# Optimization experiments

Hardware: AMD Instinct MI355X
Metric: run time of the kernel (lower is better)

The kernel has to match this reference:

```python
import jax, jax.numpy as jnp
import numpy as np

N, D, H, E, K = 16384, 1024, 4096, 8, 2
EPS = 1e-5


def setup_inputs() -> dict:
    key = jax.random.key(0)
    ks = jax.random.split(key, 12)
    s = 0.02
    return {
        "x": jax.random.normal(ks[0], (N, D), dtype=jnp.float32),
        "ln_g": jnp.ones((D,), jnp.float32),
        "ln_b": jnp.zeros((D,), jnp.float32),
        "r_w1": jax.random.normal(ks[1], (D, H // 2), jnp.float32) * s,
        "r_b1": jnp.zeros((H // 2,), jnp.float32),
        "r_w2": jax.random.normal(ks[2], (H // 2, E), jnp.float32) * s,
        "r_b2": jnp.zeros((E,), jnp.float32),
        "e_w1": jax.random.normal(ks[3], (E, D, H), jnp.float32) * s,
        "e_b1": jnp.zeros((E, H), jnp.float32),
        "e_w2": jax.random.normal(ks[4], (E, H, D), jnp.float32) * s,
        "e_b2": jnp.zeros((E, D), jnp.float32),
    }


def reference(x, ln_g, ln_b, r_w1, r_b1, r_w2, r_b2, e_w1, e_b1, e_w2, e_b2):
    # LayerNorm
    mu = jnp.mean(x, axis=-1, keepdims=True)
    var = jnp.mean(jnp.square(x - mu), axis=-1, keepdims=True)
    xn = (x - mu) * jax.lax.rsqrt(var + EPS) * ln_g + ln_b  # [N, D]

    # Router: Linear -> ReLU -> Linear -> softmax -> top-k, renormalize
    logits = jax.nn.relu(xn @ r_w1 + r_b1) @ r_w2 + r_b2  # [N, E]
    probs = jax.nn.softmax(logits, axis=-1)
    vals, idx = jax.lax.top_k(probs, K)  # [N, K]
    vals = vals / jnp.sum(vals, axis=-1, keepdims=True)

    # Dense expert dispatch: loop over fixed small E, weight by combine gate
    out = jnp.zeros_like(x)
    for e in range(E):
        gate = jnp.sum(vals * (idx == e).astype(vals.dtype), axis=-1)  # [N]
        h = jax.nn.relu(xn @ e_w1[e] + e_b1[e])  # dropout in eval mode -> identity
        y = h @ e_w2[e] + e_b2[e]  # [N, D]
        out = out + gate[:, None] * y
    return x + out
```

## Files before the change

kernel.cpp:

```cpp
#include <hip/hip_runtime.h>
#include <cstdint>
#include <cstddef>

typedef unsigned short u16;
typedef __attribute__((ext_vector_type(8))) short bf16x8;
typedef __attribute__((ext_vector_type(4))) float f32x4;

#define N_TOK 16384
#define DIM   1024
#define HID   4096
#define NEXP  8
#define HR    2048
#define TAU   0.02f
#define MAXMT 264
#define MAXMT2 136

__device__ __forceinline__ u16 f2bf(float f) {
  union { float f; uint32_t u; } x; x.f = f;
  uint32_t r = x.u + 0x7FFFu + ((x.u >> 16) & 1u);
  return (u16)(r >> 16);
}
__device__ __forceinline__ float bf2f(u16 u) {
  union { uint32_t u; float f; } x; x.u = ((uint32_t)u) << 16; return x.f;
}

__device__ __forceinline__ void async16(const void* g, const void* l) {
  auto gp = reinterpret_cast<const __attribute__((address_space(1))) uint32_t*>(
      reinterpret_cast<uintptr_t>(g));
  auto lp = reinterpret_cast<__attribute__((address_space(3))) uint32_t*>(
      reinterpret_cast<uintptr_t>(l));
  __builtin_amdgcn_global_load_lds(gp, lp, 16, 0, 0);
}

__device__ __forceinline__ unsigned xcd_swz(unsigned flat, unsigned nwg) {
  const unsigned xcd = flat & 7u, lid = flat >> 3;
  const unsigned q = nwg >> 3, r = nwg & 7u;
  return (xcd < r ? xcd * (q + 1u) : r * (q + 1u) + (xcd - r) * q) + lid;
}

template<bool SPLIT>
__global__ __launch_bounds__(256)
void transpose_cvt(const float* __restrict__ src, u16* __restrict__ hi,
                   u16* __restrict__ lo, int R, int C)
{
  __shared__ float tile[64][65];
  const size_t bofs = (size_t)blockIdx.z * R * C;
  src += bofs; hi += bofs; if (SPLIT) lo += bofs;
  const int t = threadIdx.x;
  const int c0 = blockIdx.x * 64, r0 = blockIdx.y * 64;
#pragma unroll
  for (int i = 0; i < 4; ++i) {
    const int idx = i * 256 + t;
    const int rr = idx >> 4;
    const int cc = (idx & 15) << 2;
    const float4 v = *(const float4*)(src + (size_t)(r0 + rr) * C + c0 + cc);
    tile[rr][cc] = v.x; tile[rr][cc + 1] = v.y;
    tile[rr][cc + 2] = v.z; tile[rr][cc + 3] = v.w;
  }
  __syncthreads();
#pragma unroll
  for (int i = 0; i < 4; ++i) {
    const int idx = i * 256 + t;
    const int oc = idx >> 4;
    const int rc = (idx & 15) << 2;
    float v0 = tile[rc][oc], v1 = tile[rc + 1][oc];
    float v2 = tile[rc + 2][oc], v3 = tile[rc + 3][oc];
    ushort4 h;
    h.x = f2bf(v0); h.y = f2bf(v1); h.z = f2bf(v2); h.w = f2bf(v3);
    const size_t o = (size_t)(c0 + oc) * R + r0 + rc;
    *(ushort4*)(hi + o) = h;
    if (SPLIT) {
      ushort4 l;
      l.x = f2bf(v0 - bf2f(h.x)); l.y = f2bf(v1 - bf2f(h.y));
      l.z = f2bf(v2 - bf2f(h.z)); l.w = f2bf(v3 - bf2f(h.w));
      *(ushort4*)(lo + o) = l;
    }
  }
}

__global__ __launch_bounds__(256)
void ln_kernel(const float* __restrict__ x, const float* __restrict__ g,
               const float* __restrict__ b, u16* __restrict__ xh,
               u16* __restrict__ xl, float* __restrict__ out)
{
  const int row = blockIdx.x;
  const int t = threadIdx.x;
  const float4 xv = ((const float4*)(x + (size_t)row * DIM))[t];
  float s = xv.x + xv.y + xv.z + xv.w;
  float q = xv.x * xv.x + xv.y * xv.y + xv.z * xv.z + xv.w * xv.w;
#pragma unroll
  for (int off = 32; off; off >>= 1) {
    s += __shfl_down(s, off, 64);
    q += __shfl_down(q, off, 64);
  }
  __shared__ float sm[8];
  __shared__ float mu_s, rs_s;
  const int lane = t & 63, wv = t >> 6;
  if (lane == 0) { sm[wv] = s; sm[wv + 4] = q; }
  __syncthreads();
  if (t == 0) {
    float S = sm[0] + sm[1] + sm[2] + sm[3];
    float Q = sm[4] + sm[5] + sm[6] + sm[7];
    float mu = S * (1.f / DIM);
    float var = Q * (1.f / DIM) - mu * mu;
    mu_s = mu; rs_s = rsqrtf(var + 1e-5f);
  }
  __syncthreads();
  const float mu = mu_s, rs = rs_s;
  const float4 gv = ((const float4*)g)[t];
  const float4 bv = ((const float4*)b)[t];
  float n0 = (xv.x - mu) * rs * gv.x + bv.x;
  float n1 = (xv.y - mu) * rs * gv.y + bv.y;
  float n2 = (xv.z - mu) * rs * gv.z + bv.z;
  float n3 = (xv.w - mu) * rs * gv.w + bv.w;
  ushort4 h, l;
  h.x = f2bf(n0); l.x = f2bf(n0 - bf2f(h.x));
  h.y = f2bf(n1); l.y = f2bf(n1 - bf2f(h.y));
  h.z = f2bf(n2); l.z = f2bf(n2 - bf2f(h.z));
  h.w = f2bf(n3); l.w = f2bf(n3 - bf2f(h.w));
  ((ushort4*)(xh + (size_t)row * DIM))[t] = h;
  ((ushort4*)(xl + (size_t)row * DIM))[t] = l;
  ((float4*)(out + (size_t)row * DIM))[t] = xv;
}

__global__ __launch_bounds__(256)
void logits_kernel(const u16* __restrict__ HrB, const float* __restrict__ w2,
                   float* __restrict__ logits)
{
  const int row = blockIdx.x, t = threadIdx.x;
  const u16* h = HrB + (size_t)row * HR;
  const ushort4* hv = (const ushort4*)(h + t * 8);
  ushort4 h0 = hv[0], h1 = hv[1];
  u16 hh[8] = {h0.x, h0.y, h0.z, h0.w, h1.x, h1.y, h1.z, h1.w};
  float p[8] = {0, 0, 0, 0, 0, 0, 0, 0};
#pragma unroll
  for (int j = 0; j < 8; ++j) {
    const int col = t * 8 + j;
    const float v = bf2f(hh[j]);
    const float4* wp = (const float4*)(w2 + (size_t)col * 8);
    float4 a = wp[0], b = wp[1];
    p[0] += v * a.x; p[1] += v * a.y; p[2] += v * a.z; p[3] += v * a.w;
    p[4] += v * b.x; p[5] += v * b.y; p[6] += v * b.z; p[7] += v * b.w;
  }
#pragma unroll
  for (int off = 32; off; off >>= 1)
#pragma unroll
    for (int e = 0; e < 8; ++e) p[e] += __shfl_down(p[e], off, 64);
  __shared__ float sm[4][8];
  const int lane = t & 63, wv = t >> 6;
  if (lane == 0) {
#pragma unroll
    for (int e = 0; e < 8; ++e) sm[wv][e] = p[e];
  }
  __syncthreads();
  if (t < 8)
    logits[(size_t)row * 8 + t] = sm[0][t] + sm[1][t] + sm[2][t] + sm[3][t];
}

__device__ __forceinline__ void load_logits(const float* logits, const float* b2,
                                            int row, float l[8]) {
  const float4* lp = (const float4*)(logits + (size_t)row * 8);
  float4 a = lp[0], b = lp[1];
  l[0] = a.x + b2[0]; l[1] = a.y + b2[1]; l[2] = a.z + b2[2]; l[3] = a.w + b2[3];
  l[4] = b.x + b2[4]; l[5] = b.y + b2[5]; l[6] = b.z + b2[6]; l[7] = b.w + b2[7];
}
__device__ __forceinline__ void top2(const float l[8], int& i0, float& l0,
                                     int& i1, float& l1) {
  i0 = 0; l0 = l[0];
#pragma unroll
  for (int e = 1; e < 8; ++e) if (l[e] > l0) { l0 = l[e]; i0 = e; }
  i1 = -1; l1 = -1e30f;
#pragma unroll
  for (int e = 0; e < 8; ++e) if (e != i0 && l[e] > l1) { l1 = l[e]; i1 = e; }
}

__global__ __launch_bounds__(256)
void pass_flag(float* __restrict__ logits, const float* __restrict__ b2,
               int* __restrict__ fixL, int* __restrict__ cntFix)
{
  __shared__ int lcnt;
  __shared__ int base;
  const int t = threadIdx.x;
  const int row = blockIdx.x * 256 + t;
  if (t == 0) lcnt = 0;
  float l[8]; load_logits(logits, b2, row, l);
  int i0, i1; float l0, l1;
  top2(l, i0, l0, i1, l1);
  float l2 = -1e30f;
#pragma unroll
  for (int e = 0; e < 8; ++e)
    if (e != i0 && e != i1 && l[e] > l2) l2 = l[e];
  const bool flag = (l1 - l2) < TAU;
  __syncthreads();
  int r = 0;
  if (flag) r = atomicAdd(&lcnt, 1);
  __syncthreads();
  if (t == 0) base = atomicAdd(cntFix, lcnt);
  __syncthreads();
  if (flag) {
    fixL[base + r] = row;
    float4 z = {0.f, 0.f, 0.f, 0.f};
    ((float4*)(logits + (size_t)row * 8))[0] = z;
    ((float4*)(logits + (size_t)row * 8))[1] = z;
  }
}

__global__ __launch_bounds__(256)
void pass_count(const float* __restrict__ logits, const float* __restrict__ b2,
                int* __restrict__ cnts)
{
  __shared__ int lcnt[NEXP];
  const int t = threadIdx.x;
  const int row = blockIdx.x * 256 + t;
  if (t < NEXP) lcnt[t] = 0;
  float l[8]; load_logits(logits, b2, row, l);
  int i0, i1; float l0, l1;
  top2(l, i0, l0, i1, l1);
  __syncthreads();
  atomicAdd(&lcnt[i0], 1);
  atomicAdd(&lcnt[i1], 1);
  __syncthreads();
  if (t < NEXP) atomicAdd(&cnts[t], lcnt[t]);
}

__global__ void scan_kernel(const int* __restrict__ cnts, int* __restrict__ offs,
                            int* __restrict__ tileOffs, int* __restrict__ tileOffs2)
{
  if (threadIdx.x == 0) {
    int s = 0, ts = 0, ts2 = 0;
#pragma unroll
    for (int e = 0; e < NEXP; ++e) {
      offs[e] = s; s += cnts[e];
      tileOffs[e] = ts; ts += (cnts[e] + 127) >> 7;
      tileOffs2[e] = ts2; ts2 += (cnts[e] + 255) >> 8;
    }
    offs[NEXP] = s;
    tileOffs[NEXP] = ts;
    tileOffs2[NEXP] = ts2;
  }
}

__global__ __launch_bounds__(256)
void pass_scatter(const float* __restrict__ logits, const float* __restrict__ b2,
                  const int* __restrict__ offs, int* __restrict__ cnts2,
                  int* __restrict__ rowsC, float* __restrict__ gateC)
{
  __shared__ int lcnt[NEXP];
  __shared__ int sbase[NEXP];
  const int t = threadIdx.x;
  const int row = blockIdx.x * 256 + t;
  if (t < NEXP) lcnt[t] = 0;
  float l[8]; load_logits(logits, b2, row, l);
  int i0, i1; float l0, l1;
  top2(l, i0, l0, i1, l1);
  float tt = expf(l1 - l0);
  float g0 = 1.f / (1.f + tt);
  float g1 = tt / (1.f + tt);
  __syncthreads();
  int r0 = atomicAdd(&lcnt[i0], 1);
  int r1 = atomicAdd(&lcnt[i1], 1);
  __syncthreads();
  if (t < NEXP) sbase[t] = atomicAdd(&cnts2[t], lcnt[t]);
  __syncthreads();
  int p0 = offs[i0] + sbase[i0] + r0;
  int p1 = offs[i1] + sbase[i1] + r1;
  rowsC[p0] = row; gateC[p0] = g0;
  rowsC[p1] = row; gateC[p1] = g1;
}

#define G8_BAR() do { __builtin_amdgcn_s_barrier(); \
                      __builtin_amdgcn_sched_barrier(0); } while (0)
#define G8_VM4() asm volatile("s_waitcnt vmcnt(4)" ::: "memory")
#define G8_VM0() asm volatile("s_waitcnt vmcnt(0)" ::: "memory")
#define G8_LGKM0() do { asm volatile("s_waitcnt lgkmcnt(0)" ::: "memory"); \
                        __builtin_amdgcn_sched_barrier(0); } while (0)
#define G8_LGKM8() asm volatile("s_waitcnt lgkmcnt(8)" ::: "memory")

#define READ_A(aL, mfh, Af) do { \
  _Pragma("unroll") for (int mf = 0; mf < 4; ++mf) { \
    Af[mf][0] = *(const bf16x8*)&(aL)[((mfh)*4+mf)*1024 + aBase + swzC[0]]; \
    Af[mf][1] = *(const bf16x8*)&(aL)[((mfh)*4+mf)*1024 + aBase + swzC[1]]; \
  } } while (0)

#define READ_B(bL, nfh, Bf) do { \
  _Pragma("unroll") for (int nf = 0; nf < 2; ++nf) { \
    Bf[nf][0] = *(const bf16x8*)&(bL)[((nfh)*2+nf)*1024 + bBase + swzC[0]]; \
    Bf[nf][1] = *(const bf16x8*)&(bL)[((nfh)*2+nf)*1024 + bBase + swzC[1]]; \
  } } while (0)

#define MFMA_Q(mfh, nfh, Af, Bf) do { \
  __builtin_amdgcn_s_setprio(1); \
  _Pragma("unroll") for (int kk = 0; kk < 2; ++kk) \
  _Pragma("unroll") for (int mf = 0; mf < 4; ++mf) \
  _Pragma("unroll") for (int nf = 0; nf < 2; ++nf) \
    acc[(mfh)*4+mf][(nfh)*2+nf] = __builtin_amdgcn_mfma_f32_16x16x32_bf16( \
        Af[mf][kk], Bf[nf][kk], acc[(mfh)*4+mf][(nfh)*2+nf], 0, 0, 0); \
  __builtin_amdgcn_s_setprio(0); } while (0)

#define G8_KLOOP() do { \
  stB(0, 0); stB(0, 1); stA(0, 0); stA(0, 1); \
  stB(1, 0); stB(1, 1); \
  G8_VM4(); \
  G8_BAR(); \
  bf16x8 Af[4][2], Bf0[2][2], Bf1[2][2]; \
  const int numI = numK >> 1; \
  for (int it = 0; it < numI; ++it) { \
    const int t1 = 2 * it + 1, t2 = 2 * it + 2, t3 = 2 * it + 3; \
    const bool last = (t2 >= numK); \
    READ_A(aH[0], 0, Af); \
    READ_B(bH[0], 0, Bf0); \
    stA(t1, 0); \
    G8_LGKM8(); \
    G8_BAR(); \
    G8_LGKM0(); \
    MFMA_Q(0, 0, Af, Bf0); \
    G8_BAR(); \
    READ_B(bH[0], 1, Bf1); \
    stA(t1, 1); \
    G8_BAR(); \
    G8_LGKM0(); \
    MFMA_Q(0, 1, Af, Bf1); \
    G8_BAR(); \
    READ_A(aH[0], 1, Af); \
    if (!last) stB(t2, 0); \
    G8_BAR(); \
    G8_LGKM0(); \
    MFMA_Q(1, 1, Af, Bf1); \
    G8_BAR(); \
    if (!last) stB(t2, 1); \
    G8_BAR(); \
    MFMA_Q(1, 0, Af, Bf0); \
    if (last) { G8_VM0(); } else { G8_VM4(); } \
    G8_BAR(); \
    READ_A(aH[1], 0, Af); \
    READ_B(bH[1], 0, Bf0); \
    if (!last) stA(t2, 0); \
    G8_LGKM8(); \
    G8_BAR(); \
    G8_LGKM0(); \
    MFMA_Q(0, 0, Af, Bf0); \
    G8_BAR(); \
    READ_B(bH[1], 1, Bf1); \
    if (!last) stA(t2, 1); \
    G8_BAR(); \
    G8_LGKM0(); \
    MFMA_Q(0, 1, Af, Bf1); \
    G8_BAR(); \
    READ_A(aH[1], 1, Af); \
    if (t3 < numK) stB(t3, 0); \
    G8_BAR(); \
    G8_LGKM0(); \
    MFMA_Q(1, 1, Af, Bf1); \
    G8_BAR(); \
    if (t3 < numK) stB(t3, 1); \
    G8_BAR(); \
    MFMA_Q(1, 0, Af, Bf0); \
    if (!last) { G8_VM4(); } \
    G8_BAR(); \
  } \
} while (0)

template<int EPI>
__global__ __launch_bounds__(512, 2)
void gemm8p(const u16* __restrict__ A0, const u16* __restrict__ B0,
            int lda, int ldb, int K, int NT, int Mdense,
            const float* __restrict__ bias,
            u16* __restrict__ Cbf, int ldc)
{
  const unsigned swz = xcd_swz(blockIdx.x, gridDim.x);
  const int mt = (int)(swz / (unsigned)NT);
  if (mt >= Mdense / 256) return;
  const int m0 = mt * 256, Mq = Mdense;
  const int n0 = (int)(swz % (unsigned)NT) * 256;
  const float* bi = bias;

  __shared__ alignas(16) u16 As[2][2][128 * 64];
  __shared__ alignas(16) u16 Bs[2][2][128 * 64];

  const int t = threadIdx.x;
  const int numK = K >> 6;

  const u16* aP[2][2]; const u16* bP[2][2]; int dst[2];
#pragma unroll
  for (int j = 0; j < 2; ++j) {
    const int gdx = j * 512 + t;
    const int rw = gdx >> 3;
    const int cs = ((gdx & 7) ^ (rw & 7)) << 3;
    dst[j] = gdx * 8;
#pragma unroll
    for (int h = 0; h < 2; ++h) {
      aP[h][j] = A0 + (size_t)(m0 + h * 128 + rw) * lda + cs;
      bP[h][j] = B0 + (size_t)(n0 + h * 128 + rw) * ldb + cs;
    }
  }
  auto stA = [&](int tile, int h) {
    async16(aP[h][0] + (size_t)tile * 64, &As[tile & 1][h][dst[0]]);
    async16(aP[h][1] + (size_t)tile * 64, &As[tile & 1][h][dst[1]]);
  };
  auto stB = [&](int tile, int h) {
    async16(bP[h][0] + (size_t)tile * 64, &Bs[tile & 1][h][dst[0]]);
    async16(bP[h][1] + (size_t)tile * 64, &Bs[tile & 1][h][dst[1]]);
  };

  const int lane = t & 63, wv = t >> 6;
  const int wr = wv >> 2, wc = wv & 3;
  const int fr = lane & 15, fq = lane >> 4;
  int swzC[2];
#pragma unroll
  for (int kk = 0; kk < 2; ++kk)
    swzC[kk] = ((kk * 4 + fq) ^ (fr & 7)) << 3;
  const int aBase = fr * 64;
  const int bBase = (wc & 1) * 4096 + fr * 64;
  const u16* aH[2] = { &As[0][wr][0], &As[1][wr][0] };
  const u16* bH[2] = { &Bs[0][wc >> 1][0], &Bs[1][wc >> 1][0] };

  f32x4 acc[8][4];
#pragma unroll
  for (int i = 0; i < 8; ++i)
#pragma unroll
    for (int j = 0; j < 4; ++j) acc[i][j] = (f32x4){0.f, 0.f, 0.f, 0.f};

  G8_KLOOP();

  float bv[4];
#pragma unroll
  for (int nf = 0; nf < 4; ++nf) bv[nf] = bi[n0 + wc * 64 + nf * 16 + fr];
#pragma unroll
  for (int mf = 0; mf < 8; ++mf)
#pragma unroll
    for (int r = 0; r < 4; ++r) {
      const int m = m0 + wr * 128 + mf * 16 + fq * 4 + r;
      if (m < Mq) {
#pragma unroll
        for (int nf = 0; nf < 4; ++nf) {
          const int n = n0 + wc * 64 + nf * 16 + fr;
          Cbf[(size_t)m * ldc + n] = f2bf(fmaxf(acc[mf][nf][r] + bv[nf], 0.f));
        }
      }
    }
}

__global__ __launch_bounds__(512, 1)
void moe_fused(const u16* __restrict__ xnhi, const u16* __restrict__ ew1t,
               const u16* __restrict__ ew2t,
               const int* __restrict__ counts, const int* __restrict__ offs,
               const int* __restrict__ tileOffs2,
               const int* __restrict__ rowsC, const float* __restrict__ gatesC,
               const float* __restrict__ e_b1, const float* __restrict__ e_b2,
               u16* __restrict__ Hbuf, float* __restrict__ out,
               int* __restrict__ qc, int* __restrict__ ready)
{
  constexpr int NT1 = HID / 256;
  constexpr int NT2 = DIM / 256;
  constexpr int W1 = NT1 * MAXMT2;
  constexpr int CHA = W1 / 8;
  constexpr int CHB = (NT2 * MAXMT2) / 8;

  __shared__ alignas(16) u16 As[2][2][128 * 64];
  __shared__ alignas(16) u16 Bs[2][2][128 * 64];
  __shared__ int sh_w;

  const int t = threadIdx.x;
  const int cls = (int)(blockIdx.x & 7);
  const int lane = t & 63, wv = t >> 6;
  const int wr = wv >> 2, wc = wv & 3;
  const int fr = lane & 15, fq = lane >> 4;
  int swzC[2];
#pragma unroll
  for (int kk = 0; kk < 2; ++kk)
    swzC[kk] = ((kk * 4 + fq) ^ (fr & 7)) << 3;
  const int aBase = fr * 64;
  const int bBase = (wc & 1) * 4096 + fr * 64;
  const u16* aH[2] = { &As[0][wr][0], &As[1][wr][0] };
  const u16* bH[2] = { &Bs[0][wc >> 1][0], &Bs[1][wc >> 1][0] };

  for (;;) {
    __syncthreads();
    if (t == 0) {
      int enc = -1;
      for (int k = 0; k < 8 && enc < 0; ++k) {
        const int v = (cls + k) & 7;
        int w = atomicAdd(&qc[v], 1);
        if (w < CHA) { enc = v * CHA + w; break; }
        w = atomicAdd(&qc[8 + v], 1);
        if (w < CHB) { enc = W1 + v * CHB + w; break; }
      }
      sh_w = enc;
    }
    __syncthreads();
    const int w = sh_w;
    if (w < 0) return;
    const bool isG1 = (w < W1);
    const int wl = isG1 ? w : (w - W1);
    const int NT = isG1 ? NT1 : NT2;
    const int mt = wl / NT;
    if (mt >= tileOffs2[NEXP]) continue;
    int e = 0;
#pragma unroll
    for (int i = 1; i < NEXP; ++i) if (tileOffs2[i] <= mt) e = i;
    const int m0 = (mt - tileOffs2[e]) * 256;
    const int Mq = counts[e];
    if (m0 >= Mq) continue;
    const int off = offs[e];
    const int n0 = (wl % NT) * 256;

    if (!isG1) {
      if (t == 0) {
        while (__hip_atomic_load(ready + mt, __ATOMIC_ACQUIRE,
                                 __HIP_MEMORY_SCOPE_AGENT) < NT1)
          __builtin_amdgcn_s_sleep(8);
      }
      __syncthreads();
    }

    const int lda = isG1 ? DIM : HID;
    const int numK = (isG1 ? DIM : HID) >> 6;
    const u16* Asrc = isG1 ? xnhi : Hbuf;
    const u16* B = isG1 ? (ew1t + (size_t)e * HID * DIM)
                        : (ew2t + (size_t)e * DIM * HID);
    const float* bi = isG1 ? (e_b1 + (size_t)e * HID)
                           : (e_b2 + (size_t)e * DIM);
    const int* rows = rowsC + off;

    const u16* aP[2][2]; const u16* bP[2][2]; int dst[2];
#pragma unroll
    for (int j = 0; j < 2; ++j) {
      const int gdx = j * 512 + t;
      const int rw = gdx >> 3;
      const int cs = ((gdx & 7) ^ (rw & 7)) << 3;
      dst[j] = gdx * 8;
#pragma unroll
      for (int h = 0; h < 2; ++h) {
        const int grow = m0 + h * 128 + rw;
        const int amc = grow < Mq ? grow : (Mq - 1);
        const size_t agr = isG1 ? (size_t)rows[amc] : (size_t)(off + amc);
        aP[h][j] = Asrc + agr * lda + cs;
        bP[h][j] = B + (size_t)(n0 + h * 128 + rw) * lda + cs;
      }
    }
    auto stA = [&](int tile, int h) {
      async16(aP[h][0] + (size_t)tile * 64, &As[tile & 1][h][dst[0]]);
      async16(aP[h][1] + (size_t)tile * 64, &As[tile & 1][h][dst[1]]);
    };
    auto stB = [&](int tile, int h) {
      async16(bP[h][0] + (size_t)tile * 64, &Bs[tile & 1][h][dst[0]]);
      async16(bP[h][1] + (size_t)tile * 64, &Bs[tile & 1][h][dst[1]]);
    };

    f32x4 acc[8][4];
#pragma unroll
    for (int i = 0; i < 8; ++i)
#pragma unroll
      for (int j = 0; j < 4; ++j) acc[i][j] = (f32x4){0.f, 0.f, 0.f, 0.f};

    asm volatile("s_waitcnt vmcnt(0)" ::: "memory");

    G8_KLOOP();

    float bv[4];
#pragma unroll
    for (int nf = 0; nf < 4; ++nf) bv[nf] = bi[n0 + wc * 64 + nf * 16 + fr];

    if (isG1) {
#pragma unroll
      for (int mf = 0; mf < 8; ++mf)
#pragma unroll
        for (int r = 0; r < 4; ++r) {
          const int m = m0 + wr * 128 + mf * 16 + fq * 4 + r;
          if (m < Mq) {
#pragma unroll
            for (int nf = 0; nf < 4; ++nf) {
              const int n = n0 + wc * 64 + nf * 16 + fr;
              Hbuf[(size_t)(off + m) * HID + n] =
                  f2bf(fmaxf(acc[mf][nf][r] + bv[nf], 0.f));
            }
          }
        }
      __syncthreads();
      if (t == 0)
        __hip_atomic_fetch_add(ready + mt, 1, __ATOMIC_RELEASE,
                               __HIP_MEMORY_SCOPE_AGENT);
    } else {
#pragma unroll
      for (int mf = 0; mf < 8; ++mf)
#pragma unroll
        for (int r = 0; r < 4; ++r) {
          const int m = m0 + wr * 128 + mf * 16 + fq * 4 + r;
          if (m < Mq) {
            const size_t orow = (size_t)rows[m];
            const float g = gatesC[off + m];
#pragma unroll
            for (int nf = 0; nf < 4; ++nf) {
              const int n = n0 + wc * 64 + nf * 16 + fr;
              atomicAdd(&out[orow * DIM + n], g * (acc[mf][nf][r] + bv[nf]));
            }
          }
        }
    }
  }
}

template<bool SPLIT, int EPI, bool GATHER>
__global__ __launch_bounds__(256, 2)
void gemm_bt(const u16* __restrict__ A0, const u16* __restrict__ A1,
             const u16* __restrict__ B0, const u16* __restrict__ B1,
             int lda, int ldb, int K, int M,
             const int* __restrict__ counts, int expertArg,
             const int* __restrict__ offs,
             const int* __restrict__ rowsC, const float* __restrict__ gatesC,
             const float* __restrict__ bias,
             const float* __restrict__ w2, float* __restrict__ logits,
             u16* __restrict__ Cbf, float* __restrict__ Cf32, int ldc)
{
  int expert, m0, n0;
  if (counts == nullptr) {
    const unsigned nwg = gridDim.x * gridDim.y;
    const unsigned flat = blockIdx.y * gridDim.x + blockIdx.x;
    const unsigned swz = xcd_swz(flat, nwg);
    expert = expertArg;
    m0 = (int)(swz / gridDim.x) * 128;
    n0 = (int)(swz % gridDim.x) * 128;
  } else {
    expert = expertArg;
    m0 = blockIdx.y * 128;
    n0 = blockIdx.x * 128;
  }

  const int Mq = counts ? counts[expert] : M;
  if (m0 >= Mq) return;
  const int off = offs ? offs[expert] : 0;
  const int* rows = rowsC ? rowsC + off : nullptr;
  const float* gates = gatesC ? gatesC + off : nullptr;
  const u16* B = B0;
  const u16* Bl = SPLIT ? B1 : nullptr;
  const float* bi = bias;
  const int z = (int)blockIdx.z;
  const int zOff = z * K;

  __shared__ u16 As0[128 * 32], Bs0[128 * 32];
  __shared__ u16 As1[SPLIT ? 128 * 32 : 8], Bs1[SPLIT ? 128 * 32 : 8];

  const int t = threadIdx.x;
  size_t aoff[2]; int acodd[2]; size_t boff[2];
#pragma unroll
  for (int i = 0; i < 2; ++i) {
    int gdx = i * 256 + t;
    int ar = gdx >> 2, ac = (gdx & 3) * 8;
    int am = m0 + ar;
    int amc = am < Mq ? am : (Mq - 1);
    int agr = GATHER ? rows[amc] : amc;
    aoff[i] = (size_t)agr * lda + ac + zOff;
    boff[i] = (size_t)(n0 + ar) * ldb + ac + zOff;
    acodd[i] = gdx * 8;
  }

  f32x4 acc[4][4];
#pragma unroll
  for (int i = 0; i < 4; ++i)
#pragma unroll
    for (int j = 0; j < 4; ++j) acc[i][j] = (f32x4){0.f, 0.f, 0.f, 0.f};

  const int lane = t & 63, wv = t >> 6;
  const int wm = (wv >> 1) * 64, wn = (wv & 1) * 64;
  const int fr = lane & 15, fq = lane >> 4;

  for (int k0 = 0; k0 < K; k0 += 32) {
    __syncthreads();
#pragma unroll
    for (int i = 0; i < 2; ++i) {
      async16(A0 + aoff[i] + k0, &As0[acodd[i]]);
      async16(B + boff[i] + k0, &Bs0[acodd[i]]);
      if (SPLIT) {
        async16(A1 + aoff[i] + k0, &As1[acodd[i]]);
        async16(Bl + boff[i] + k0, &Bs1[acodd[i]]);
      }
    }
    __syncthreads();
    bf16x8 af[4], bfr[4], af1[4], bf1[4];
#pragma unroll
    for (int xi = 0; xi < 4; ++xi) {
      af[xi]  = *(const bf16x8*)&As0[(wm + xi * 16 + fr) * 32 + fq * 8];
      bfr[xi] = *(const bf16x8*)&Bs0[(wn + xi * 16 + fr) * 32 + fq * 8];
      if (SPLIT) {
        af1[xi] = *(const bf16x8*)&As1[(wm + xi * 16 + fr) * 32 + fq * 8];
        bf1[xi] = *(const bf16x8*)&Bs1[(wn + xi * 16 + fr) * 32 + fq * 8];
      }
    }
#pragma unroll
    for (int mt = 0; mt < 4; ++mt)
#pragma unroll
      for (int nt = 0; nt < 4; ++nt) {
        acc[mt][nt] = __builtin_amdgcn_mfma_f32_16x16x32_bf16(af[mt], bfr[nt], acc[mt][nt], 0, 0, 0);
        if (SPLIT) {
          acc[mt][nt] = __builtin_amdgcn_mfma_f32_16x16x32_bf16(af[mt], bf1[nt], acc[mt][nt], 0, 0, 0);
          acc[mt][nt] = __builtin_amdgcn_mfma_f32_16x16x32_bf16(af1[mt], bfr[nt], acc[mt][nt], 0, 0, 0);
        }
      }
  }

  if constexpr (EPI == 3) {
    float w2v[4][8]; float b1v[4];
#pragma unroll
    for (int nt = 0; nt < 4; ++nt) {
      const int n = n0 + wn + nt * 16 + fr;
      b1v[nt] = bi[n];
      const float4* wp = (const float4*)(w2 + (size_t)n * 8);
      float4 wa = wp[0], wb = wp[1];
      w2v[nt][0] = wa.x; w2v[nt][1] = wa.y; w2v[nt][2] = wa.z; w2v[nt][3] = wa.w;
      w2v[nt][4] = wb.x; w2v[nt][5] = wb.y; w2v[nt][6] = wb.z; w2v[nt][7] = wb.w;
    }
#pragma unroll
    for (int mt = 0; mt < 4; ++mt) {
      float pe[4][8];
#pragma unroll
      for (int r = 0; r < 4; ++r)
#pragma unroll
        for (int ee = 0; ee < 8; ++ee) pe[r][ee] = 0.f;
#pragma unroll
      for (int nt = 0; nt < 4; ++nt)
#pragma unroll
        for (int r = 0; r < 4; ++r) {
          float v = fmaxf(acc[mt][nt][r] + b1v[nt], 0.f);
#pragma unroll
          for (int ee = 0; ee < 8; ++ee) pe[r][ee] += v * w2v[nt][ee];
        }
#pragma unroll
      for (int offx = 1; offx < 16; offx <<= 1)
#pragma unroll
        for (int r = 0; r < 4; ++r)
#pragma unroll
          for (int ee = 0; ee < 8; ++ee)
            pe[r][ee] += __shfl_xor(pe[r][ee], offx, 64);
      if (fr == 0) {
#pragma unroll
        for (int r = 0; r < 4; ++r) {
          const int m = m0 + wm + mt * 16 + fq * 4 + r;
          if (m < Mq) {
            const int lrow = GATHER ? rows[m] : m;
#pragma unroll
            for (int ee = 0; ee < 8; ++ee)
              atomicAdd(&logits[(size_t)lrow * 8 + ee], pe[r][ee]);
          }
        }
      }
    }
    return;
  }

#pragma unroll
  for (int mt = 0; mt < 4; ++mt) {
#pragma unroll
    for (int nt = 0; nt < 4; ++nt) {
      const int n = n0 + wn + nt * 16 + fr;
      const float bvv = (z == 0) ? bi[n] : 0.f;
#pragma unroll
      for (int r = 0; r < 4; ++r) {
        const int m = m0 + wm + mt * 16 + fq * 4 + r;
        if (m < Mq) {
          float v = acc[mt][nt][r] + bvv;
          if constexpr (EPI == 1) {
            Cbf[(size_t)m * ldc + n] = f2bf(fmaxf(v, 0.f));
          } else {
            atomicAdd(&Cf32[(size_t)rows[m] * ldc + n], gates[m] * v);
          }
        }
      }
    }
  }
}

extern "C" void kernel_launch(void* const* d_in, const int* in_sizes, int n_in,
                              void* d_out, int out_size, void* d_ws, size_t ws_size,
                              hipStream_t stream)
{
  const float* x    = (const float*)d_in[0];
  const float* ln_g = (const float*)d_in[1];
  const float* ln_b = (const float*)d_in[2];
  const float* r_w1 = (const float*)d_in[3];
  const float* r_b1 = (const float*)d_in[4];
  const float* r_w2 = (const float*)d_in[5];
  const float* r_b2 = (const float*)d_in[6];
  const float* e_w1 = (const float*)d_in[7];
  const float* e_b1 = (const float*)d_in[8];
  const float* e_w2 = (const float*)d_in[9];
  const float* e_b2 = (const float*)d_in[10];
  float* out = (float*)d_out;

  char* ws = (char*)d_ws;
  const size_t MB = 1024ull * 1024ull;
  u16*   xnhi = (u16*)(ws);
  u16*   xnlo = (u16*)(ws + 32 * MB);
  u16*   rw1h = (u16*)(ws + 64 * MB);
  u16*   rw1l = (u16*)(ws + 68 * MB);
  u16*   ew1t = (u16*)(ws + 72 * MB);
  u16*   ew2t = (u16*)(ws + 136 * MB);
  float* logits = (float*)(ws + 200 * MB);
  int*   rowsC  = (int*)(ws + 200 * MB + 512 * 1024);
  float* gateC  = (float*)(ws + 200 * MB + 640 * 1024);
  int*   fixL   = (int*)(ws + 200 * MB + 768 * 1024);
  int*   cntb   = (int*)(ws + 200 * MB + 832 * 1024);
  int*   cnts   = cntb;
  int*   cnts2  = cntb + 8;
  int*   offs   = cntb + 16;
  int*   cntFix = cntb + 25;
  int*   tileOffs  = cntb + 32;
  int*   tileOffs2 = cntb + 48;
  int*   qready = (int*)(ws + 200 * MB + 836 * 1024);
  int*   qc     = qready;
  int*   ready  = qready + 16;
  u16*   Hbuf = (u16*)(ws + 201 * MB);
  u16*   HrB  = Hbuf;
  (void)in_sizes; (void)n_in; (void)out_size;

  const bool fused = ws_size >= 458ull * MB;

  hipMemsetAsync(cntb, 0, 256, stream);
  hipMemsetAsync(qready, 0, 4096, stream);

  transpose_cvt<true ><<<dim3(HR / 64, DIM / 64, 1), 256, 0, stream>>>(r_w1, rw1h, rw1l, DIM, HR);
  transpose_cvt<false><<<dim3(HID / 64, DIM / 64, NEXP), 256, 0, stream>>>(e_w1, ew1t, nullptr, DIM, HID);
  transpose_cvt<false><<<dim3(DIM / 64, HID / 64, NEXP), 256, 0, stream>>>(e_w2, ew2t, nullptr, HID, DIM);

  ln_kernel<<<N_TOK, 256, 0, stream>>>(x, ln_g, ln_b, xnhi, xnlo, out);

  gemm8p<1><<<dim3((HR / 256) * (N_TOK / 256)), 512, 0, stream>>>(
      xnhi, rw1h, DIM, DIM, DIM, HR / 256, N_TOK, r_b1, HrB, HR);

  logits_kernel<<<N_TOK, 256, 0, stream>>>(HrB, r_w2, logits);

  pass_flag<<<N_TOK / 256, 256, 0, stream>>>(logits, r_b2, fixL, cntFix);

  gemm_bt<true, 3, true><<<dim3(HR / 128, N_TOK / 128), 256, 0, stream>>>(
      xnhi, xnlo, rw1h, rw1l, DIM, DIM, DIM, N_TOK,
      cntFix, 0, nullptr, fixL, nullptr, r_b1, r_w2, logits,
      nullptr, nullptr, 0);

  pass_count<<<N_TOK / 256, 256, 0, stream>>>(logits, r_b2, cnts);
  scan_kernel<<<1, 64, 0, stream>>>(cnts, offs, tileOffs, tileOffs2);
  pass_scatter<<<N_TOK / 256, 256, 0, stream>>>(logits, r_b2, offs, cnts2, rowsC, gateC);

  if (fused) {
    moe_fused<<<dim3(256), 512, 0, stream>>>(
        xnhi, ew1t, ew2t, cnts, offs, tileOffs2, rowsC, gateC,
        e_b1, e_b2, Hbuf, out, qc, ready);
  } else {
    for (int e = 0; e < NEXP; ++e) {
      gemm_bt<false, 1, true><<<dim3(HID / 128, N_TOK / 128), 256, 0, stream>>>(
          xnhi, nullptr, ew1t + (size_t)e * HID * DIM, nullptr,
          DIM, DIM, DIM, N_TOK,
          cnts, e, offs, rowsC, nullptr, e_b1 + (size_t)e * HID, nullptr, nullptr,
          Hbuf, nullptr, HID);
      gemm_bt<false, 2, false><<<dim3(DIM / 128, N_TOK / 128, 2), 256, 0, stream>>>(
          Hbuf, nullptr, ew2t + (size_t)e * DIM * HID, nullptr,
          HID, HID, HID / 2, N_TOK,
          cnts, e, offs, rowsC, gateC, e_b2 + (size_t)e * DIM, nullptr, nullptr,
          nullptr, out, DIM);
    }
  }
}
```

Measured before the change: 1.368 ms.

## Fuse router second linear into first GEMM epilogue with atomic logit accumulation

The router's first GEMM no longer writes the ReLU hidden activations to global memory in bf16 for a separate logits kernel to read back. Its epilogue now multiplies the ReLU output by r_w2 in registers, reduces across lanes with shuffles, and atomically adds partial logits per row, with logits zeroed beforehand. This removes a 64MB write plus read and one kernel launch. In exchange it adds float atomics with 8-way contention per logit, nondeterministic summation order, a heavier register epilogue (launch bounds drop to 1 block), and logits computed from fp32 rather than bf16-rounded hidden values, which can change top-2 choices near ties.

Measured after the change: 1.746 ms. 1.28x slower.

```diff
diff --git a/kernel.cpp b/kernel.cpp
--- a/kernel.cpp
+++ b/kernel.cpp
@@ -123,40 +123,6 @@
   ((float4*)(out + (size_t)row * DIM))[t] = xv;
 }
 
-__global__ __launch_bounds__(256)
-void logits_kernel(const u16* __restrict__ HrB, const float* __restrict__ w2,
-                   float* __restrict__ logits)
-{
-  const int row = blockIdx.x, t = threadIdx.x;
-  const u16* h = HrB + (size_t)row * HR;
-  const ushort4* hv = (const ushort4*)(h + t * 8);
-  ushort4 h0 = hv[0], h1 = hv[1];
-  u16 hh[8] = {h0.x, h0.y, h0.z, h0.w, h1.x, h1.y, h1.z, h1.w};
-  float p[8] = {0, 0, 0, 0, 0, 0, 0, 0};
-#pragma unroll
-  for (int j = 0; j < 8; ++j) {
-    const int col = t * 8 + j;
-    const float v = bf2f(hh[j]);
-    const float4* wp = (const float4*)(w2 + (size_t)col * 8);
-    float4 a = wp[0], b = wp[1];
-    p[0] += v * a.x; p[1] += v * a.y; p[2] += v * a.z; p[3] += v * a.w;
-    p[4] += v * b.x; p[5] += v * b.y; p[6] += v * b.z; p[7] += v * b.w;
-  }
-#pragma unroll
-  for (int off = 32; off; off >>= 1)
-#pragma unroll
-    for (int e = 0; e < 8; ++e) p[e] += __shfl_down(p[e], off, 64);
-  __shared__ float sm[4][8];
-  const int lane = t & 63, wv = t >> 6;
-  if (lane == 0) {
-#pragma unroll
-    for (int e = 0; e < 8; ++e) sm[wv][e] = p[e];
-  }
-  __syncthreads();
-  if (t < 8)
-    logits[(size_t)row * 8 + t] = sm[0][t] + sm[1][t] + sm[2][t] + sm[3][t];
-}
-
 __device__ __forceinline__ void load_logits(const float* logits, const float* b2,
                                             int row, float l[8]) {
   const float4* lp = (const float4*)(logits + (size_t)row * 8);
@@ -360,25 +326,23 @@
   } \
 } while (0)
 
-template<int EPI>
-__global__ __launch_bounds__(512, 2)
-void gemm8p(const u16* __restrict__ A0, const u16* __restrict__ B0,
-            int lda, int ldb, int K, int NT, int Mdense,
-            const float* __restrict__ bias,
-            u16* __restrict__ Cbf, int ldc)
-{
+__global__ __launch_bounds__(512, 1)
+void gemm8p_router(const u16* __restrict__ A0, const u16* __restrict__ B0,
+                   const float* __restrict__ b1, const float* __restrict__ w2,
+                   float* __restrict__ logits)
+{
+  const int NT = HR / 256;
   const unsigned swz = xcd_swz(blockIdx.x, gridDim.x);
   const int mt = (int)(swz / (unsigned)NT);
-  if (mt >= Mdense / 256) return;
-  const int m0 = mt * 256, Mq = Mdense;
+  if (mt >= N_TOK / 256) return;
+  const int m0 = mt * 256;
   const int n0 = (int)(swz % (unsigned)NT) * 256;
-  const float* bi = bias;
 
   __shared__ alignas(16) u16 As[2][2][128 * 64];
   __shared__ alignas(16) u16 Bs[2][2][128 * 64];
 
   const int t = threadIdx.x;
-  const int numK = K >> 6;
+  const int numK = DIM >> 6;
 
   const u16* aP[2][2]; const u16* bP[2][2]; int dst[2];
 #pragma unroll
@@ -389,8 +353,8 @@
     dst[j] = gdx * 8;
 #pragma unroll
     for (int h = 0; h < 2; ++h) {
-      aP[h][j] = A0 + (size_t)(m0 + h * 128 + rw) * lda + cs;
-      bP[h][j] = B0 + (size_t)(n0 + h * 128 + rw) * ldb + cs;
+      aP[h][j] = A0 + (size_t)(m0 + h * 128 + rw) * DIM + cs;
+      bP[h][j] = B0 + (size_t)(n0 + h * 128 + rw) * DIM + cs;
     }
   }
   auto stA = [&](int tile, int h) {
@@ -422,22 +386,48 @@
 
   G8_KLOOP();
 
-  float bv[4];
-#pragma unroll
-  for (int nf = 0; nf < 4; ++nf) bv[nf] = bi[n0 + wc * 64 + nf * 16 + fr];
-#pragma unroll
-  for (int mf = 0; mf < 8; ++mf)
-#pragma unroll
-    for (int r = 0; r < 4; ++r) {
-      const int m = m0 + wr * 128 + mf * 16 + fq * 4 + r;
-      if (m < Mq) {
-#pragma unroll
-        for (int nf = 0; nf < 4; ++nf) {
-          const int n = n0 + wc * 64 + nf * 16 + fr;
-          Cbf[(size_t)m * ldc + n] = f2bf(fmaxf(acc[mf][nf][r] + bv[nf], 0.f));
-        }
-      }
-    }
+  float bv[4]; float w2v[4][8];
+#pragma unroll
+  for (int nf = 0; nf < 4; ++nf) {
+    const int n = n0 + wc * 64 + nf * 16 + fr;
+    bv[nf] = b1[n];
+    const float4* wp = (const float4*)(w2 + (size_t)n * 8);
+    float4 wa = wp[0], wb = wp[1];
+    w2v[nf][0] = wa.x; w2v[nf][1] = wa.y; w2v[nf][2] = wa.z; w2v[nf][3] = wa.w;
+    w2v[nf][4] = wb.x; w2v[nf][5] = wb.y; w2v[nf][6] = wb.z; w2v[nf][7] = wb.w;
+  }
+#pragma unroll
+  for (int mf = 0; mf < 8; ++mf) {
+    float pe[4][8];
+#pragma unroll
+    for (int r = 0; r < 4; ++r)
+#pragma unroll
+      for (int e = 0; e < 8; ++e) pe[r][e] = 0.f;
+#pragma unroll
+    for (int nf = 0; nf < 4; ++nf)
+#pragma unroll
+      for (int r = 0; r < 4; ++r) {
+        const float v = fmaxf(acc[mf][nf][r] + bv[nf], 0.f);
+#pragma unroll
+        for (int e = 0; e < 8; ++e) pe[r][e] += v * w2v[nf][e];
+      }
+#pragma unroll
+    for (int offx = 1; offx < 16; offx <<= 1)
+#pragma unroll
+      for (int r = 0; r < 4; ++r)
+#pragma unroll
+        for (int e = 0; e < 8; ++e)
+          pe[r][e] += __shfl_xor(pe[r][e], offx, 64);
+    if (fr == 0) {
+#pragma unroll
+      for (int r = 0; r < 4; ++r) {
+        const int m = m0 + wr * 128 + mf * 16 + fq * 4 + r;
+#pragma unroll
+        for (int e = 0; e < 8; ++e)
+          atomicAdd(&logits[(size_t)m * 8 + e], pe[r][e]);
+      }
+    }
+  }
 }
 
 __global__ __launch_bounds__(512, 1)
@@ -809,13 +799,13 @@
   int*   qc     = qready;
   int*   ready  = qready + 16;
   u16*   Hbuf = (u16*)(ws + 201 * MB);
-  u16*   HrB  = Hbuf;
   (void)in_sizes; (void)n_in; (void)out_size;
 
   const bool fused = ws_size >= 458ull * MB;
 
   hipMemsetAsync(cntb, 0, 256, stream);
   hipMemsetAsync(qready, 0, 4096, stream);
+  hipMemsetAsync(logits, 0, 512 * 1024, stream);
 
   transpose_cvt<true ><<<dim3(HR / 64, DIM / 64, 1), 256, 0, stream>>>(r_w1, rw1h, rw1l, DIM, HR);
   transpose_cvt<false><<<dim3(HID / 64, DIM / 64, NEXP), 256, 0, stream>>>(e_w1, ew1t, nullptr, DIM, HID);
@@ -823,10 +813,8 @@
 
   ln_kernel<<<N_TOK, 256, 0, stream>>>(x, ln_g, ln_b, xnhi, xnlo, out);
 
-  gemm8p<1><<<dim3((HR / 256) * (N_TOK / 256)), 512, 0, stream>>>(
-      xnhi, rw1h, DIM, DIM, DIM, HR / 256, N_TOK, r_b1, HrB, HR);
-
-  logits_kernel<<<N_TOK, 256, 0, stream>>>(HrB, r_w2, logits);
+  gemm8p_router<<<dim3((HR / 256) * (N_TOK / 256)), 512, 0, stream>>>(
+      xnhi, rw1h, r_b1, r_w2, logits);
 
   pass_flag<<<N_TOK / 256, 256, 0, stream>>>(logits, r_b2, fixL, cntFix);
 
```
